# Performance work log

Measured on AMD Instinct MI355X. Metric: run time of the kernel, lower is better.

The kernel has to match this reference:

```python
import jax, jax.numpy as jnp
import numpy as np

B, T, C = 2, 2048, 1024
H, KVH = 16, 4
HD = C // H  # 64
EPS = 1e-6


def _rope_tables(t, half, base=10000.0):
    inv_freq = 1.0 / (base ** (np.arange(0, half, dtype=np.float32) / half))
    ang = np.arange(t, dtype=np.float32)[:, None] * inv_freq[None, :]
    return jnp.asarray(np.cos(ang)), jnp.asarray(np.sin(ang))


def setup_inputs() -> dict:
    key = jax.random.key(0)
    ks = jax.random.split(key, 5)
    cos, sin = _rope_tables(T, HD // 2)
    return {
        "x": jax.random.normal(ks[0], (B, T, C), dtype=jnp.float32),
        "cos": cos,
        "sin": sin,
        "Wq": jax.random.normal(ks[1], (C, H * HD), dtype=jnp.float32) * 0.02,
        "Wk": jax.random.normal(ks[2], (C, KVH * HD), dtype=jnp.float32) * 0.02,
        "Wv": jax.random.normal(ks[3], (C, KVH * HD), dtype=jnp.float32) * 0.02,
        "Wo": jax.random.normal(ks[4], (H * HD, C), dtype=jnp.float32) * 0.02,
    }


def _apply_rope(x, cos, sin):
    # x: (B, h, T, HD); cos/sin: (T, HD//2) broadcast over batch/heads
    d = x.shape[-1] // 2
    x1, x2 = x[..., :d], x[..., d:]
    c = cos[None, None, :, :]
    s = sin[None, None, :, :]
    return jnp.concatenate([x1 * c + x2 * s, -x1 * s + x2 * c], axis=-1)


def _rmsnorm(x):
    return x * jax.lax.rsqrt(jnp.mean(x * x, axis=-1, keepdims=True) + EPS)


def reference(x, cos, sin, Wq, Wk, Wv, Wo):
    q = (x @ Wq).reshape(B, T, H, HD).transpose(0, 2, 1, 3)      # (B,H,T,HD)
    k = (x @ Wk).reshape(B, T, KVH, HD).transpose(0, 2, 1, 3)    # (B,KVH,T,HD)
    v = (x @ Wv).reshape(B, T, KVH, HD).transpose(0, 2, 1, 3)
    q = _rmsnorm(_apply_rope(q, cos, sin))
    k = _rmsnorm(_apply_rope(k, cos, sin))
    # GQA: group query heads onto kv heads
    G = H // KVH
    qg = q.reshape(B, KVH, G, T, HD)
    scores = jnp.einsum('bkgqd,bksd->bkgqs', qg, k) / jnp.sqrt(jnp.asarray(HD, x.dtype))
    causal = jnp.tril(jnp.ones((T, T), dtype=bool))
    scores = jnp.where(causal[None, None, None], scores, jnp.finfo(x.dtype).min)
    p = jax.nn.softmax(scores, axis=-1)
    y = jnp.einsum('bkgqs,bksd->bkgqd', p, v)                    # (B,KVH,G,T,HD)
    y = y.reshape(B, H, T, HD).transpose(0, 2, 1, 3).reshape(B, T, H * HD)
    return y @ Wo
```

## Files before the change

kernel.cpp:

```cpp
#include <hip/hip_runtime.h>
#include <hip/hip_bf16.h>

#define Bb  2
#define Tt  2048
#define Cc  1024
#define Hh  16
#define KVH 4
#define HD  64

typedef __attribute__((ext_vector_type(4))) float  f32x4;
typedef __attribute__((ext_vector_type(8))) __bf16 bf16x8;

typedef __attribute__((address_space(1))) const unsigned int glob_u32;
typedef __attribute__((address_space(3))) unsigned int       lds_u32;

__device__ __forceinline__ void gload16(const void* g, void* l) {
  __builtin_amdgcn_global_load_lds((glob_u32*)g, (lds_u32*)l, 16, 0, 0);
}

__device__ __forceinline__ unsigned short f2bf_bits(float f) {
  unsigned int u = __builtin_bit_cast(unsigned int, f);
  u = (u + 0x7fff + ((u >> 16) & 1)) >> 16;
  return (unsigned short)u;
}

__global__ __launch_bounds__(256) void cast_x_kernel(const float* __restrict__ in,
                                                     unsigned short* __restrict__ out, int n) {
  int i = (blockIdx.x * 256 + threadIdx.x) * 4;
  if (i >= n) return;
  float4 f = *(const float4*)(in + i);
  unsigned long long v = (unsigned long long)f2bf_bits(f.x)
                       | ((unsigned long long)f2bf_bits(f.y) << 16)
                       | ((unsigned long long)f2bf_bits(f.z) << 32)
                       | ((unsigned long long)f2bf_bits(f.w) << 48);
  *(unsigned long long*)(out + i) = v;
}

__global__ __launch_bounds__(256) void transpose_cast(const float* __restrict__ W,
                                                      unsigned short* __restrict__ Wt,
                                                      int K, int N) {
  __shared__ float tile[32][33];
  int k0 = blockIdx.x * 32, n0 = blockIdx.y * 32;
  int tx = threadIdx.x;
  for (int i = threadIdx.y; i < 32; i += 8)
    tile[i][tx] = W[(size_t)(k0 + i) * N + n0 + tx];
  __syncthreads();
  for (int i = threadIdx.y; i < 32; i += 8)
    Wt[(size_t)(n0 + i) * K + k0 + tx] = f2bf_bits(tile[tx][i]);
}

__global__ __launch_bounds__(256) void gemm_bf16(const unsigned short* __restrict__ A,
                                                 const unsigned short* __restrict__ Bt,
                                                 float* __restrict__ C,
                                                 int M, int N, int K, int ldc) {
  __shared__ unsigned short As[128 * 32];
  __shared__ unsigned short Bs[128 * 32];
  const int tid = threadIdx.x;
  const int wave = tid >> 6, lane = tid & 63;
  const int row0 = blockIdx.x * 128;
  const int col0 = blockIdx.y * 128;
  const int wm = (wave >> 1) * 64, wn = (wave & 1) * 64;
  f32x4 acc[4][4];
#pragma unroll
  for (int m = 0; m < 4; ++m)
#pragma unroll
    for (int n = 0; n < 4; ++n) acc[m][n] = (f32x4){0.f, 0.f, 0.f, 0.f};

  for (int k0 = 0; k0 < K; k0 += 32) {
#pragma unroll
    for (int c = 0; c < 2; ++c) {
      int chunk = wave * 2 + c;
      int r = chunk * 16 + (lane >> 2);
      int kc = (lane & 3) * 8;
      gload16(A + (size_t)(row0 + r) * K + k0 + kc, (void*)(As + chunk * 512));
      gload16(Bt + (size_t)(col0 + r) * K + k0 + kc, (void*)(Bs + chunk * 512));
    }
    __syncthreads();
    bf16x8 af[4], bfr[4];
#pragma unroll
    for (int m = 0; m < 4; ++m)
      af[m] = *(const bf16x8*)&As[(wm + m * 16 + (lane & 15)) * 32 + (lane >> 4) * 8];
#pragma unroll
    for (int n = 0; n < 4; ++n)
      bfr[n] = *(const bf16x8*)&Bs[(wn + n * 16 + (lane & 15)) * 32 + (lane >> 4) * 8];
#pragma unroll
    for (int m = 0; m < 4; ++m)
#pragma unroll
      for (int n = 0; n < 4; ++n)
        acc[m][n] = __builtin_amdgcn_mfma_f32_16x16x32_bf16(af[m], bfr[n], acc[m][n], 0, 0, 0);
    __syncthreads();
  }
#pragma unroll
  for (int m = 0; m < 4; ++m)
#pragma unroll
    for (int n = 0; n < 4; ++n) {
      int col = col0 + wn + n * 16 + (lane & 15);
      int rbase = row0 + wm + m * 16 + (lane >> 4) * 4;
#pragma unroll
      for (int i = 0; i < 4; ++i)
        C[(size_t)(rbase + i) * ldc + col] = acc[m][n][i];
    }
}

__global__ __launch_bounds__(256) void rope_rms_kernel(const float* __restrict__ QKV,
                                                       const float* __restrict__ cosT,
                                                       const float* __restrict__ sinT,
                                                       unsigned short* __restrict__ Qb,
                                                       unsigned short* __restrict__ Kb,
                                                       unsigned short* __restrict__ Vb) {
  int wid = blockIdx.x * 4 + (threadIdx.x >> 6);
  int lane = threadIdx.x & 63;
  int slot = wid % 24;
  int bt = wid / 24;
  int b = bt >> 11;
  int t = bt & 2047;
  const float* base = QKV + (size_t)bt * 1536;
  if (slot < 20) {
    bool isQ = slot < 16;
    int hh = isQ ? slot : (slot - 16);
    float v = base[(isQ ? hh * 64 : 1024 + hh * 64) + lane];
    float other = __shfl_xor(v, 32);
    int d = lane & 31;
    float c = cosT[t * 32 + d], sn = sinT[t * 32 + d];
    float o = (lane < 32) ? (v * c + other * sn) : (v * c - other * sn);
    float ss = o * o;
    ss += __shfl_xor(ss, 1);  ss += __shfl_xor(ss, 2);
    ss += __shfl_xor(ss, 4);  ss += __shfl_xor(ss, 8);
    ss += __shfl_xor(ss, 16); ss += __shfl_xor(ss, 32);
    float scale = rsqrtf(ss * (1.f / 64.f) + 1e-6f);
    if (isQ) scale *= 0.125f;
    unsigned short ob = f2bf_bits(o * scale);
    if (isQ) Qb[((size_t)(b * Hh + hh) * Tt + t) * 64 + lane] = ob;
    else     Kb[((size_t)(b * KVH + hh) * Tt + t) * 64 + lane] = ob;
  } else {
    int vh = slot - 20;
    float v = base[1280 + vh * 64 + lane];
    Vb[((size_t)(b * KVH + vh) * Tt + t) * 64 + lane] = f2bf_bits(v);
  }
}

__global__ __launch_bounds__(256) void attn_kernel(const unsigned short* __restrict__ Qb,
                                                   const unsigned short* __restrict__ Kb,
                                                   const unsigned short* __restrict__ Vb,
                                                   unsigned short* __restrict__ Yb) {
  __shared__ unsigned short Ks[64 * 64];
  __shared__ unsigned short Vs[64 * 64];
  __shared__ unsigned short Ps[4 * 16 * 64];
  const int tid = threadIdx.x, wave = tid >> 6, lane = tid & 63;
  const int bid = blockIdx.x;
  const int qtile = 31 - (bid & 31);
  const int bh = bid >> 5;
  const int b = bh >> 4, h = bh & 15;
  const int kvh = h >> 2;
  const int q0 = qtile * 64;
  const size_t qbase = (size_t)(b * Hh + h) * Tt * 64;
  const size_t kbase = (size_t)(b * KVH + kvh) * Tt * 64;

  bf16x8 qf[2];
  {
    int qrow = q0 + wave * 16 + (lane & 15);
    const unsigned short* qp = Qb + qbase + (size_t)qrow * 64 + (lane >> 4) * 8;
    qf[0] = *(const bf16x8*)qp;
    qf[1] = *(const bf16x8*)(qp + 32);
  }
  f32x4 acc[4];
  float m_r[4], l_r[4];
#pragma unroll
  for (int n = 0; n < 4; ++n) acc[n] = (f32x4){0.f, 0.f, 0.f, 0.f};
#pragma unroll
  for (int i = 0; i < 4; ++i) { m_r[i] = -INFINITY; l_r[i] = 0.f; }

  char* PsW = (char*)Ps + wave * 2048;

  const int ntiles = qtile + 1;
  for (int t = 0; t < ntiles; ++t) {
#pragma unroll
    for (int c = 0; c < 2; ++c) {
      int chunk = wave * 2 + c;
      int r = chunk * 8 + (lane >> 3);
      int bcol = ((lane & 7) * 16) ^ ((r & 7) << 4);
      size_t g = (size_t)(t * 64 + r) * 64 + (bcol >> 1);
      gload16(Kb + kbase + g, (void*)(Ks + chunk * 512));
      gload16(Vb + kbase + g, (void*)(Vs + chunk * 512));
    }
    __syncthreads();
    f32x4 s[4];
#pragma unroll
    for (int n = 0; n < 4; ++n) {
      f32x4 z = (f32x4){0.f, 0.f, 0.f, 0.f};
#pragma unroll
      for (int st = 0; st < 2; ++st) {
        int krow = n * 16 + (lane & 15);
        int kb = ((lane >> 4) * 16 + st * 64) ^ ((krow & 7) << 4);
        bf16x8 kf = *(const bf16x8*)((const char*)Ks + krow * 128 + kb);
        z = __builtin_amdgcn_mfma_f32_16x16x32_bf16(qf[st], kf, z, 0, 0, 0);
      }
      s[n] = z;
    }
    if (t == qtile) {
#pragma unroll
      for (int n = 0; n < 4; ++n)
#pragma unroll
        for (int i = 0; i < 4; ++i) {
          int kcol = t * 64 + n * 16 + (lane & 15);
          int qrow = q0 + wave * 16 + (lane >> 4) * 4 + i;
          if (kcol > qrow) s[n][i] = -INFINITY;
        }
    }
#pragma unroll
    for (int i = 0; i < 4; ++i) {
      float rmax = fmaxf(fmaxf(s[0][i], s[1][i]), fmaxf(s[2][i], s[3][i]));
      rmax = fmaxf(rmax, __shfl_xor(rmax, 1));
      rmax = fmaxf(rmax, __shfl_xor(rmax, 2));
      rmax = fmaxf(rmax, __shfl_xor(rmax, 4));
      rmax = fmaxf(rmax, __shfl_xor(rmax, 8));
      float mn = fmaxf(m_r[i], rmax);
      float corr = __expf(m_r[i] - mn);
      m_r[i] = mn;
      float rsum = 0.f;
      int prow = (lane >> 4) * 4 + i;
#pragma unroll
      for (int n = 0; n < 4; ++n) {
        float p = __expf(s[n][i] - mn);
        rsum += p;
        int cb = ((n * 16 + (lane & 15)) * 2) ^ ((prow & 7) << 4);
        *(unsigned short*)(PsW + prow * 128 + cb) = f2bf_bits(p);
      }
      rsum += __shfl_xor(rsum, 1);
      rsum += __shfl_xor(rsum, 2);
      rsum += __shfl_xor(rsum, 4);
      rsum += __shfl_xor(rsum, 8);
      l_r[i] = l_r[i] * corr + rsum;
#pragma unroll
      for (int n = 0; n < 4; ++n) acc[n][i] *= corr;
    }
    asm volatile("s_waitcnt lgkmcnt(0)" ::: "memory");
#pragma unroll
    for (int n = 0; n < 4; ++n) {
#pragma unroll
      for (int st = 0; st < 2; ++st) {
        int prow = lane & 15;
        int pb = ((lane >> 4) * 16 + st * 64) ^ ((prow & 7) << 4);
        bf16x8 pf = *(const bf16x8*)((const char*)PsW + prow * 128 + pb);
        union { bf16x8 v; unsigned short u[8]; } vf;
#pragma unroll
        for (int j = 0; j < 8; ++j) {
          int kv = st * 32 + (lane >> 4) * 8 + j;
          int db = ((n * 16 + (lane & 15)) * 2) ^ ((kv & 7) << 4);
          vf.u[j] = *(const unsigned short*)((const char*)Vs + kv * 128 + db);
        }
        acc[n] = __builtin_amdgcn_mfma_f32_16x16x32_bf16(pf, vf.v, acc[n], 0, 0, 0);
      }
    }
    __syncthreads();
  }
#pragma unroll
  for (int n = 0; n < 4; ++n)
#pragma unroll
    for (int i = 0; i < 4; ++i) {
      int qrow = q0 + wave * 16 + (lane >> 4) * 4 + i;
      int col = h * 64 + n * 16 + (lane & 15);
      float v = acc[n][i] / l_r[i];
      Yb[(size_t)(b * Tt + qrow) * 1024 + col] = f2bf_bits(v);
    }
}

extern "C" void kernel_launch(void* const* d_in, const int* in_sizes, int n_in,
                              void* d_out, int out_size, void* d_ws, size_t ws_size,
                              hipStream_t stream) {
  const float* x    = (const float*)d_in[0];
  const float* cosT = (const float*)d_in[1];
  const float* sinT = (const float*)d_in[2];
  const float* Wq   = (const float*)d_in[3];
  const float* Wk   = (const float*)d_in[4];
  const float* Wv   = (const float*)d_in[5];
  const float* Wo   = (const float*)d_in[6];
  float* out = (float*)d_out;
  char* ws = (char*)d_ws;

  unsigned short* xb    = (unsigned short*)(ws);
  unsigned short* Wqkvt = (unsigned short*)(ws + 8388608);
  unsigned short* Wot   = (unsigned short*)(ws + 11534336);
  float*          QKV   = (float*)(ws + 13631488);
  unsigned short* Qb    = (unsigned short*)(ws + 38797312);
  unsigned short* Kb    = (unsigned short*)(ws + 47185920);
  unsigned short* Vb    = (unsigned short*)(ws + 49283072);
  unsigned short* Yb    = (unsigned short*)(ws + 51380224);

  cast_x_kernel<<<4096, 256, 0, stream>>>(x, xb, Bb * Tt * Cc);
  transpose_cast<<<dim3(32, 32), dim3(32, 8), 0, stream>>>(Wq, Wqkvt, 1024, 1024);
  transpose_cast<<<dim3(32, 8),  dim3(32, 8), 0, stream>>>(Wk, Wqkvt + 1024 * 1024, 1024, 256);
  transpose_cast<<<dim3(32, 8),  dim3(32, 8), 0, stream>>>(Wv, Wqkvt + 1280 * 1024, 1024, 256);
  transpose_cast<<<dim3(32, 32), dim3(32, 8), 0, stream>>>(Wo, Wot, 1024, 1024);

  gemm_bf16<<<dim3(32, 12), 256, 0, stream>>>(xb, Wqkvt, QKV, 4096, 1536, 1024, 1536);
  rope_rms_kernel<<<24576, 256, 0, stream>>>(QKV, cosT, sinT, Qb, Kb, Vb);
  attn_kernel<<<1024, 256, 0, stream>>>(Qb, Kb, Vb, Yb);
  gemm_bf16<<<dim3(32, 8), 256, 0, stream>>>(Yb, Wot, out, 4096, 1024, 1024, 1024);
}
```

Before: 305.3 us.

## Double-buffer K/V tiles in attention and pre-transpose V for vectorized reads

Adds a v_transpose kernel that writes V as bf16 in a head-dim-major layout. With that layout the PV MFMA operand can be read from LDS as 16-byte vectors instead of eight scalar 2-byte loads per fragment. The attention loop now double-buffers K and V tiles in LDS, issuing the next tile's global-to-LDS loads right after the barrier so they overlap compute. One of the two barriers per iteration is removed. The cost is an extra kernel launch, a transpose pass through shared memory, and twice the LDS for K/V, which may reduce occupancy.

Result: faster. 269.9 us (-11.6%).

```diff
diff --git a/kernel.cpp b/kernel.cpp
--- a/kernel.cpp
+++ b/kernel.cpp
@@ -106,45 +106,57 @@
                                                        const float* __restrict__ cosT,
                                                        const float* __restrict__ sinT,
                                                        unsigned short* __restrict__ Qb,
-                                                       unsigned short* __restrict__ Kb,
-                                                       unsigned short* __restrict__ Vb) {
+                                                       unsigned short* __restrict__ Kb) {
   int wid = blockIdx.x * 4 + (threadIdx.x >> 6);
   int lane = threadIdx.x & 63;
-  int slot = wid % 24;
-  int bt = wid / 24;
+  int slot = wid % 20;
+  int bt = wid / 20;
   int b = bt >> 11;
   int t = bt & 2047;
   const float* base = QKV + (size_t)bt * 1536;
-  if (slot < 20) {
-    bool isQ = slot < 16;
-    int hh = isQ ? slot : (slot - 16);
-    float v = base[(isQ ? hh * 64 : 1024 + hh * 64) + lane];
-    float other = __shfl_xor(v, 32);
-    int d = lane & 31;
-    float c = cosT[t * 32 + d], sn = sinT[t * 32 + d];
-    float o = (lane < 32) ? (v * c + other * sn) : (v * c - other * sn);
-    float ss = o * o;
-    ss += __shfl_xor(ss, 1);  ss += __shfl_xor(ss, 2);
-    ss += __shfl_xor(ss, 4);  ss += __shfl_xor(ss, 8);
-    ss += __shfl_xor(ss, 16); ss += __shfl_xor(ss, 32);
-    float scale = rsqrtf(ss * (1.f / 64.f) + 1e-6f);
-    if (isQ) scale *= 0.125f;
-    unsigned short ob = f2bf_bits(o * scale);
-    if (isQ) Qb[((size_t)(b * Hh + hh) * Tt + t) * 64 + lane] = ob;
-    else     Kb[((size_t)(b * KVH + hh) * Tt + t) * 64 + lane] = ob;
-  } else {
-    int vh = slot - 20;
-    float v = base[1280 + vh * 64 + lane];
-    Vb[((size_t)(b * KVH + vh) * Tt + t) * 64 + lane] = f2bf_bits(v);
-  }
+  bool isQ = slot < 16;
+  int hh = isQ ? slot : (slot - 16);
+  float v = base[(isQ ? hh * 64 : 1024 + hh * 64) + lane];
+  float other = __shfl_xor(v, 32);
+  int d = lane & 31;
+  float c = cosT[t * 32 + d], sn = sinT[t * 32 + d];
+  float o = (lane < 32) ? (v * c + other * sn) : (v * c - other * sn);
+  float ss = o * o;
+  ss += __shfl_xor(ss, 1);  ss += __shfl_xor(ss, 2);
+  ss += __shfl_xor(ss, 4);  ss += __shfl_xor(ss, 8);
+  ss += __shfl_xor(ss, 16); ss += __shfl_xor(ss, 32);
+  float scale = rsqrtf(ss * (1.f / 64.f) + 1e-6f);
+  if (isQ) scale *= 0.125f;
+  unsigned short ob = f2bf_bits(o * scale);
+  if (isQ) Qb[((size_t)(b * Hh + hh) * Tt + t) * 64 + lane] = ob;
+  else     Kb[((size_t)(b * KVH + hh) * Tt + t) * 64 + lane] = ob;
+}
+
+__global__ __launch_bounds__(256) void v_transpose(const float* __restrict__ QKV,
+                                                   unsigned short* __restrict__ Vt) {
+  __shared__ float tile[64][65];
+  const int tid = threadIdx.x;
+  const int bid = blockIdx.x;
+  const int ttile = bid & 31;
+  const int head = bid >> 5;
+  const int b = head >> 2, vh = head & 3;
+  const int t0 = ttile * 64;
+  const int tx = tid & 63, ty = tid >> 6;
+  const size_t inbase = ((size_t)(b * Tt + t0)) * 1536 + 1280 + vh * 64;
+  for (int i = ty; i < 64; i += 4)
+    tile[i][tx] = QKV[inbase + (size_t)i * 1536 + tx];
+  __syncthreads();
+  const size_t outbase = (size_t)head * 64 * 2048 + t0;
+  for (int i = ty; i < 64; i += 4)
+    Vt[outbase + (size_t)i * 2048 + tx] = f2bf_bits(tile[tx][i]);
 }
 
 __global__ __launch_bounds__(256) void attn_kernel(const unsigned short* __restrict__ Qb,
                                                    const unsigned short* __restrict__ Kb,
-                                                   const unsigned short* __restrict__ Vb,
+                                                   const unsigned short* __restrict__ Vt,
                                                    unsigned short* __restrict__ Yb) {
-  __shared__ unsigned short Ks[64 * 64];
-  __shared__ unsigned short Vs[64 * 64];
+  __shared__ unsigned short Ks[2][64 * 64];
+  __shared__ unsigned short Vs[2][64 * 64];
   __shared__ unsigned short Ps[4 * 16 * 64];
   const int tid = threadIdx.x, wave = tid >> 6, lane = tid & 63;
   const int bid = blockIdx.x;
@@ -155,6 +167,13 @@
   const int q0 = qtile * 64;
   const size_t qbase = (size_t)(b * Hh + h) * Tt * 64;
   const size_t kbase = (size_t)(b * KVH + kvh) * Tt * 64;
+  const size_t vbase = (size_t)(b * KVH + kvh) * 64 * 2048;
+
+  const int chunk0 = wave * 2;
+  const int sr0 = chunk0 * 8 + (lane >> 3);
+  const int sr1 = sr0 + 8;
+  const int sb0 = ((lane & 7) * 16) ^ ((sr0 & 7) << 4);
+  const int sb1 = ((lane & 7) * 16) ^ ((sr1 & 7) << 4);
 
   bf16x8 qf[2];
   {
@@ -173,17 +192,25 @@
   char* PsW = (char*)Ps + wave * 2048;
 
   const int ntiles = qtile + 1;
+  {
+    gload16(Kb + kbase + (size_t)sr0 * 64 + (sb0 >> 1), (void*)(Ks[0] + chunk0 * 512));
+    gload16(Vt + vbase + (size_t)sr0 * 2048 + (sb0 >> 1), (void*)(Vs[0] + chunk0 * 512));
+    gload16(Kb + kbase + (size_t)sr1 * 64 + (sb1 >> 1), (void*)(Ks[0] + chunk0 * 512 + 512));
+    gload16(Vt + vbase + (size_t)sr1 * 2048 + (sb1 >> 1), (void*)(Vs[0] + chunk0 * 512 + 512));
+  }
+
   for (int t = 0; t < ntiles; ++t) {
-#pragma unroll
-    for (int c = 0; c < 2; ++c) {
-      int chunk = wave * 2 + c;
-      int r = chunk * 8 + (lane >> 3);
-      int bcol = ((lane & 7) * 16) ^ ((r & 7) << 4);
-      size_t g = (size_t)(t * 64 + r) * 64 + (bcol >> 1);
-      gload16(Kb + kbase + g, (void*)(Ks + chunk * 512));
-      gload16(Vb + kbase + g, (void*)(Vs + chunk * 512));
-    }
+    const int cur = t & 1;
     __syncthreads();
+    if (t + 1 < ntiles) {
+      const int nxt = cur ^ 1;
+      const size_t kt = kbase + (size_t)(t + 1) * 64 * 64;
+      const size_t vt = vbase + (size_t)(t + 1) * 64;
+      gload16(Kb + kt + (size_t)sr0 * 64 + (sb0 >> 1), (void*)(Ks[nxt] + chunk0 * 512));
+      gload16(Vt + vt + (size_t)sr0 * 2048 + (sb0 >> 1), (void*)(Vs[nxt] + chunk0 * 512));
+      gload16(Kb + kt + (size_t)sr1 * 64 + (sb1 >> 1), (void*)(Ks[nxt] + chunk0 * 512 + 512));
+      gload16(Vt + vt + (size_t)sr1 * 2048 + (sb1 >> 1), (void*)(Vs[nxt] + chunk0 * 512 + 512));
+    }
     f32x4 s[4];
 #pragma unroll
     for (int n = 0; n < 4; ++n) {
@@ -192,7 +219,7 @@
       for (int st = 0; st < 2; ++st) {
         int krow = n * 16 + (lane & 15);
         int kb = ((lane >> 4) * 16 + st * 64) ^ ((krow & 7) << 4);
-        bf16x8 kf = *(const bf16x8*)((const char*)Ks + krow * 128 + kb);
+        bf16x8 kf = *(const bf16x8*)((const char*)Ks[cur] + krow * 128 + kb);
         z = __builtin_amdgcn_mfma_f32_16x16x32_bf16(qf[st], kf, z, 0, 0, 0);
       }
       s[n] = z;
@@ -235,24 +262,19 @@
       for (int n = 0; n < 4; ++n) acc[n][i] *= corr;
     }
     asm volatile("s_waitcnt lgkmcnt(0)" ::: "memory");
-#pragma unroll
-    for (int n = 0; n < 4; ++n) {
-#pragma unroll
-      for (int st = 0; st < 2; ++st) {
-        int prow = lane & 15;
-        int pb = ((lane >> 4) * 16 + st * 64) ^ ((prow & 7) << 4);
-        bf16x8 pf = *(const bf16x8*)((const char*)PsW + prow * 128 + pb);
-        union { bf16x8 v; unsigned short u[8]; } vf;
-#pragma unroll
-        for (int j = 0; j < 8; ++j) {
-          int kv = st * 32 + (lane >> 4) * 8 + j;
-          int db = ((n * 16 + (lane & 15)) * 2) ^ ((kv & 7) << 4);
-          vf.u[j] = *(const unsigned short*)((const char*)Vs + kv * 128 + db);
-        }
-        acc[n] = __builtin_amdgcn_mfma_f32_16x16x32_bf16(pf, vf.v, acc[n], 0, 0, 0);
+    {
+      int prow = lane & 15;
+      bf16x8 pf0 = *(const bf16x8*)((const char*)PsW + prow * 128 + (((lane >> 4) * 16 + 0)  ^ ((prow & 7) << 4)));
+      bf16x8 pf1 = *(const bf16x8*)((const char*)PsW + prow * 128 + (((lane >> 4) * 16 + 64) ^ ((prow & 7) << 4)));
+#pragma unroll
+      for (int n = 0; n < 4; ++n) {
+        int d = n * 16 + (lane & 15);
+        bf16x8 vf0 = *(const bf16x8*)((const char*)Vs[cur] + d * 128 + (((lane >> 4) * 16 + 0)  ^ ((d & 7) << 4)));
+        bf16x8 vf1 = *(const bf16x8*)((const char*)Vs[cur] + d * 128 + (((lane >> 4) * 16 + 64) ^ ((d & 7) << 4)));
+        acc[n] = __builtin_amdgcn_mfma_f32_16x16x32_bf16(pf0, vf0, acc[n], 0, 0, 0);
+        acc[n] = __builtin_amdgcn_mfma_f32_16x16x32_bf16(pf1, vf1, acc[n], 0, 0, 0);
       }
     }
-    __syncthreads();
   }
 #pragma unroll
   for (int n = 0; n < 4; ++n)
@@ -284,7 +306,7 @@
   float*          QKV   = (float*)(ws + 13631488);
   unsigned short* Qb    = (unsigned short*)(ws + 38797312);
   unsigned short* Kb    = (unsigned short*)(ws + 47185920);
-  unsigned short* Vb    = (unsigned short*)(ws + 49283072);
+  unsigned short* Vt    = (unsigned short*)(ws + 49283072);
   unsigned short* Yb    = (unsigned short*)(ws + 51380224);
 
   cast_x_kernel<<<4096, 256, 0, stream>>>(x, xb, Bb * Tt * Cc);
@@ -294,7 +316,8 @@
   transpose_cast<<<dim3(32, 32), dim3(32, 8), 0, stream>>>(Wo, Wot, 1024, 1024);
 
   gemm_bf16<<<dim3(32, 12), 256, 0, stream>>>(xb, Wqkvt, QKV, 4096, 1536, 1024, 1536);
-  rope_rms_kernel<<<24576, 256, 0, stream>>>(QKV, cosT, sinT, Qb, Kb, Vb);
-  attn_kernel<<<1024, 256, 0, stream>>>(Qb, Kb, Vb, Yb);
+  rope_rms_kernel<<<20480, 256, 0, stream>>>(QKV, cosT, sinT, Qb, Kb);
+  v_transpose<<<256, 256, 0, stream>>>(QKV, Vt);
+  attn_kernel<<<1024, 256, 0, stream>>>(Qb, Kb, Vt, Yb);
   gemm_bf16<<<dim3(32, 8), 256, 0, stream>>>(Yb, Wot, out, 4096, 1024, 1024, 1024);
 }
```
